# Kernel optimization log

Hardware: AMD Instinct MI355X
Metric: run time of the kernel (lower is better)

The kernel has to match this reference:

```python
import jax, jax.numpy as jnp
import numpy as np

N_NODES = 100000
N_EDGES = 3200000
F_IN = 256
H = 256
L = 256
BN_EPS = 1e-5


def gcn_conv(x, src, dst, deg_inv_sqrt, W, b):
    # x: [N, Fin]; src/dst: [E+N] (self-loops appended); returns [N, Fout]
    h = x @ W  # dense transform first (Fout may be < Fin)
    norm = deg_inv_sqrt[src] * deg_inv_sqrt[dst]  # [E+N]
    msg = h[src] * norm[:, None]                  # gather
    out = jax.ops.segment_sum(msg, dst, num_segments=N_NODES)  # scatter-add
    return out + b


def batch_norm(x, gamma, beta):
    # BatchNorm1d in training mode: per-feature mean/var over the node dim
    mean = jnp.mean(x, axis=0)
    var = jnp.var(x, axis=0)
    return (x - mean) * jax.lax.rsqrt(var + BN_EPS) * gamma + beta


def setup_inputs() -> dict:
    key = jax.random.key(0)
    ks = jax.random.split(key, 8)
    x = jax.random.normal(ks[0], (N_NODES, F_IN), dtype=jnp.float32)
    edge_index = jax.random.randint(ks[1], (2, N_EDGES), 0, N_NODES, dtype=jnp.int64)
    # glorot-ish init for weights
    W1 = jax.random.normal(ks[2], (F_IN, H), dtype=jnp.float32) * (1.0 / np.sqrt(F_IN))
    b1 = jnp.zeros((H,), dtype=jnp.float32)
    W_mu = jax.random.normal(ks[3], (H, L), dtype=jnp.float32) * (1.0 / np.sqrt(H))
    b_mu = jnp.zeros((L,), dtype=jnp.float32)
    W_ls = jax.random.normal(ks[4], (H, L), dtype=jnp.float32) * (1.0 / np.sqrt(H))
    b_ls = jnp.zeros((L,), dtype=jnp.float32)
    gamma = jnp.ones((H,), dtype=jnp.float32)
    beta = jnp.zeros((H,), dtype=jnp.float32)
    return {"x": x, "edge_index": edge_index, "W1": W1, "b1": b1,
            "W_mu": W_mu, "b_mu": b_mu, "W_ls": W_ls, "b_ls": b_ls,
            "gamma": gamma, "beta": beta}


def reference(x, edge_index, W1, b1, W_mu, b_mu, W_ls, b_ls, gamma, beta):
    # Add self-loops once (shared across the three GCNConv layers)
    loop = jnp.arange(N_NODES, dtype=edge_index.dtype)
    src = jnp.concatenate([edge_index[0], loop])
    dst = jnp.concatenate([edge_index[1], loop])
    deg = jax.ops.segment_sum(jnp.ones_like(dst, dtype=jnp.float32), dst,
                              num_segments=N_NODES)
    deg_inv_sqrt = jnp.where(deg > 0, jax.lax.rsqrt(jnp.maximum(deg, 1.0)), 0.0)

    h = gcn_conv(x, src, dst, deg_inv_sqrt, W1, b1)
    h = jax.nn.relu(batch_norm(h, gamma, beta))
    mu = gcn_conv(h, src, dst, deg_inv_sqrt, W_mu, b_mu)
    logstd = gcn_conv(h, src, dst, deg_inv_sqrt, W_ls, b_ls)
    return (mu, logstd)
```

## Files before the change

kernel.cpp:

```cpp
#include <hip/hip_runtime.h>
#include <hip/hip_bf16.h>

#define FEAT 256
#define NPB 512
#define NPB_SHIFT 9
#define MAXBINS 256
#define CAP 20480
#define BIN_CHUNK 8192

typedef __attribute__((ext_vector_type(8))) short bf16x8;
typedef __attribute__((ext_vector_type(8))) ushort u16x8;
typedef __attribute__((ext_vector_type(4))) float f32x4;

__device__ __forceinline__ float bf2f(ushort h) {
    union { unsigned u; float f; } v; v.u = ((unsigned)h) << 16; return v.f;
}
__device__ __forceinline__ ushort f2bf(float f) {
    union { float f; unsigned u; } v; v.f = f;
    unsigned u = v.u;
    return (ushort)((u + 0x7FFFu + ((u >> 16) & 1u)) >> 16);
}


__global__ __launch_bounds__(256) void k_bin(const int* __restrict__ ei, int E, int N,
                                             int* __restrict__ bincur,
                                             int2* __restrict__ binbuf, int nbins,
                                             int nchunks,
                                             const float* __restrict__ W1,
                                             const float* __restrict__ Wmu,
                                             const float* __restrict__ Wls,
                                             const float* __restrict__ bmu,
                                             const float* __restrict__ bls,
                                             ushort* __restrict__ Wt1,
                                             ushort* __restrict__ Wtc,
                                             float* __restrict__ biasc,
                                             float* __restrict__ bnacc) {
    int t = threadIdx.x;
    if ((int)blockIdx.x >= nchunks) {
        int i = ((int)blockIdx.x - nchunks) * 256 + t;
        int m = i >> 16;
        int j = i & 65535;
        int n = j >> 8, k = j & 255;
        const float* W = (m == 0) ? W1 : (m == 1) ? Wmu : Wls;
        ushort v = f2bf(W[k * 256 + n]);
        if (m == 0) Wt1[j] = v;
        else if (m == 1) Wtc[j] = v;
        else Wtc[65536 + j] = v;
        if (i < 512) { biasc[i] = (i < 256) ? bmu[i] : bls[i - 256]; bnacc[i] = 0.f; }
        return;
    }
    __shared__ int hist[MAXBINS];
    __shared__ int base[MAXBINS];
    int T = E + N;
    int start = blockIdx.x * BIN_CHUNK;
    int end = min(start + BIN_CHUNK, T);
    for (int b = t; b < nbins; b += 256) hist[b] = 0;
    __syncthreads();
    for (int idx = start + t; idx < end; idx += 256) {
        int d = (idx < E) ? ei[E + idx] : idx - E;
        atomicAdd(&hist[d >> NPB_SHIFT], 1);
    }
    __syncthreads();
    for (int b = t; b < nbins; b += 256) {
        int c = hist[b];
        base[b] = c ? (b * CAP + atomicAdd(&bincur[b], c)) : 0;
        hist[b] = 0;
    }
    __syncthreads();
    for (int idx = start + t; idx < end; idx += 256) {
        int s, d;
        if (idx < E) { s = ei[idx]; d = ei[E + idx]; }
        else         { s = idx - E; d = idx - E; }
        int b = d >> NPB_SHIFT;
        int local = atomicAdd(&hist[b], 1);
        binbuf[base[b] + local] = make_int2(s, d);
    }
}


__global__ __launch_bounds__(512) void k_histcsr(const int2* __restrict__ binbuf,
                                                 const int* __restrict__ bincur,
                                                 int* __restrict__ offs,
                                                 float* __restrict__ dis,
                                                 int* __restrict__ csr,
                                                 const float* __restrict__ x,
                                                 ushort* __restrict__ xtab,
                                                 int N, int nbins) {
    __shared__ int bsh[256];
    __shared__ int h[NPB];
    __shared__ int cur[NPB];
    __shared__ float sdis[NPB];
    int b = blockIdx.x;
    int t = threadIdx.x;
    int node0 = b * NPB;
    int nn = min(NPB, N - node0);
    if (t < 256) bsh[t] = (t < nbins) ? bincur[t] : 0;
    h[t] = 0; cur[t] = 0;
    __syncthreads();
    for (int d = 1; d < 256; d <<= 1) {
        int xx = (t < 256 && t >= d) ? bsh[t - d] : 0;
        __syncthreads();
        if (t < 256) bsh[t] += xx;
        __syncthreads();
    }
    int cnt = bincur[b];
    int bpre = bsh[b] - cnt;
    if (b == 0 && t == 0) offs[N] = bsh[nbins - 1];
    int base = b * CAP;
    for (int i = t; i < cnt; i += 512) {
        atomicAdd(&h[binbuf[base + i].y - node0], 1);
    }
    __syncthreads();
    int v = h[t];
    for (int d = 1; d < 512; d <<= 1) {
        int xx = (t >= d) ? h[t - d] : 0;
        __syncthreads();
        h[t] += xx;
        __syncthreads();
    }
    int myoff = bpre + h[t] - v;
    float dv = rsqrtf((float)v);
    sdis[t] = dv;
    if (t < nn) {
        offs[node0 + t] = myoff;
        dis[node0 + t] = dv;
    }
    h[t] = myoff;
    __syncthreads();
    for (int i = t; i < cnt; i += 512) {
        int2 e = binbuf[base + i];
        int ld = e.y - node0;
        int c = atomicAdd(&cur[ld], 1);
        csr[h[ld] + c] = e.x;
    }
    const float4* x4 = (const float4*)x;
    ushort4* y4 = (ushort4*)xtab;
    for (int i = t; i < nn * 64; i += 512) {
        int ln = i >> 6;
        int c = i & 63;
        float d = sdis[ln];
        float4 vv = x4[(size_t)(node0 + ln) * 64 + c];
        ushort4 o;
        o.x = f2bf(vv.x * d); o.y = f2bf(vv.y * d);
        o.z = f2bf(vv.z * d); o.w = f2bf(vv.w * d);
        y4[(size_t)(node0 + ln) * 64 + c] = o;
    }
}


__global__ __launch_bounds__(256) void k_agg(const ushort* __restrict__ in,
                                             ushort* __restrict__ out,
                                             const int* __restrict__ offs,
                                             const int* __restrict__ csr,
                                             const float* __restrict__ dis, int N) {
    int wid = blockIdx.x * 4 + ((int)threadIdx.x >> 6);
    if (wid >= N) return;
    int lane = threadIdx.x & 63;
    int half = lane >> 5;
    int l32 = lane & 31;
    int beg = offs[wid], end = offs[wid + 1];
    float acc[8] = {};
    int k = beg;
    for (; k + 16 <= end; k += 16) {
        int s0 = csr[k + half];
        int s1 = csr[k + 2 + half];
        int s2 = csr[k + 4 + half];
        int s3 = csr[k + 6 + half];
        int s4 = csr[k + 8 + half];
        int s5 = csr[k + 10 + half];
        int s6 = csr[k + 12 + half];
        int s7 = csr[k + 14 + half];
        bf16x8 v0 = *(const bf16x8*)(in + (size_t)s0 * FEAT + l32 * 8);
        bf16x8 v1 = *(const bf16x8*)(in + (size_t)s1 * FEAT + l32 * 8);
        bf16x8 v2 = *(const bf16x8*)(in + (size_t)s2 * FEAT + l32 * 8);
        bf16x8 v3 = *(const bf16x8*)(in + (size_t)s3 * FEAT + l32 * 8);
        bf16x8 v4 = *(const bf16x8*)(in + (size_t)s4 * FEAT + l32 * 8);
        bf16x8 v5 = *(const bf16x8*)(in + (size_t)s5 * FEAT + l32 * 8);
        bf16x8 v6 = *(const bf16x8*)(in + (size_t)s6 * FEAT + l32 * 8);
        bf16x8 v7 = *(const bf16x8*)(in + (size_t)s7 * FEAT + l32 * 8);
        #pragma unroll
        for (int j = 0; j < 8; ++j) {
            float t0 = bf2f((ushort)v0[j]) + bf2f((ushort)v1[j]);
            float t1 = bf2f((ushort)v2[j]) + bf2f((ushort)v3[j]);
            float t2 = bf2f((ushort)v4[j]) + bf2f((ushort)v5[j]);
            float t3 = bf2f((ushort)v6[j]) + bf2f((ushort)v7[j]);
            acc[j] += (t0 + t1) + (t2 + t3);
        }
    }
    for (; k + 2 <= end; k += 2) {
        int s = csr[k + half];
        bf16x8 v = *(const bf16x8*)(in + (size_t)s * FEAT + l32 * 8);
        #pragma unroll
        for (int j = 0; j < 8; ++j) acc[j] += bf2f((ushort)v[j]);
    }
    if (k < end && half == 0) {
        int s = csr[k];
        bf16x8 v = *(const bf16x8*)(in + (size_t)s * FEAT + l32 * 8);
        #pragma unroll
        for (int j = 0; j < 8; ++j) acc[j] += bf2f((ushort)v[j]);
    }
    #pragma unroll
    for (int j = 0; j < 8; ++j) acc[j] += __shfl_xor(acc[j], 32, 64);
    if (half == 0) {
        float d = dis[wid];
        u16x8 o;
        #pragma unroll
        for (int j = 0; j < 8; ++j) o[j] = f2bf(acc[j] * d);
        *(u16x8*)(out + (size_t)wid * FEAT + l32 * 8) = o;
    }
}


template <int NCOL, bool BF16OUT>
__global__ __launch_bounds__(512) void k_gemm(const ushort* __restrict__ A,
                                              const ushort* __restrict__ Bt,
                                              const float* __restrict__ bias,
                                              float* __restrict__ C0,
                                              float* __restrict__ C1,
                                              ushort* __restrict__ Cb,
                                              float* __restrict__ bnacc,
                                              int M) {
    __shared__ ushort As[128 * 64];
    __shared__ ushort Bs[256 * 64];
    int t = threadIdx.x;
    int lane = t & 63;
    int wave = t >> 6;
    int wr = wave >> 2, wc = wave & 3;
    int bx = blockIdx.x, by = blockIdx.y;
    int lo = lane & 15, g = lane >> 4;
    f32x4 acc[4][4] = {};
    int chunk = t & 7;
    int row8 = t >> 3;

    for (int kt = 0; kt < 4; ++kt) {
        int k0 = kt * 64;
        #pragma unroll
        for (int i = 0; i < 2; ++i) {
            int r = row8 + i * 64;
            int lc = chunk ^ (r & 7);
            int gr = by * 128 + r;
            bf16x8 av = {};
            if (gr < M) av = *(const bf16x8*)(A + (size_t)gr * 256 + k0 + lc * 8);
            *(bf16x8*)(As + r * 64 + chunk * 8) = av;
        }
        #pragma unroll
        for (int i = 0; i < 4; ++i) {
            int r = row8 + i * 64;
            int lc = chunk ^ (r & 7);
            int gn = bx * 256 + r;
            bf16x8 bv = *(const bf16x8*)(Bt + (size_t)gn * 256 + k0 + lc * 8);
            *(bf16x8*)(Bs + r * 64 + chunk * 8) = bv;
        }
        __syncthreads();
        #pragma unroll
        for (int h = 0; h < 2; ++h) {
            bf16x8 af[4], bfr[4];
            #pragma unroll
            for (int m = 0; m < 4; ++m) {
                int r = wr * 64 + m * 16 + lo;
                af[m] = *(const bf16x8*)(As + r * 64 + (((h * 4 + g) ^ (r & 7)) * 8));
            }
            #pragma unroll
            for (int n = 0; n < 4; ++n) {
                int r = wc * 64 + n * 16 + lo;
                bfr[n] = *(const bf16x8*)(Bs + r * 64 + (((h * 4 + g) ^ (r & 7)) * 8));
            }
            #pragma unroll
            for (int m = 0; m < 4; ++m)
                #pragma unroll
                for (int n = 0; n < 4; ++n)
                    acc[m][n] = __builtin_amdgcn_mfma_f32_16x16x32_bf16(
                        af[m], bfr[n], acc[m][n], 0, 0, 0);
        }
        __syncthreads();
    }
    #pragma unroll
    for (int n = 0; n < 4; ++n) {
        int gc = bx * 256 + wc * 64 + n * 16 + lo;
        float bb = bias[gc];
        float s = 0.f, q = 0.f;
        #pragma unroll
        for (int m = 0; m < 4; ++m) {
            f32x4 v = acc[m][n];
            #pragma unroll
            for (int r4 = 0; r4 < 4; ++r4) {
                int grow = by * 128 + wr * 64 + m * 16 + g * 4 + r4;
                if (grow < M) {
                    float val = v[r4] + bb;
                    if (BF16OUT) {
                        Cb[(size_t)grow * 256 + gc] = f2bf(val);
                        s += val; q += val * val;
                    } else {
                        float* Cp = C0; int cc = gc;
                        if (gc >= 256) { Cp = C1; cc = gc - 256; }
                        __builtin_nontemporal_store(val, &Cp[(size_t)grow * 256 + cc]);
                    }
                }
            }
        }
        if (BF16OUT) {
            s += __shfl_xor(s, 16, 64); s += __shfl_xor(s, 32, 64);
            q += __shfl_xor(q, 16, 64); q += __shfl_xor(q, 32, 64);
            if (g == 0) {
                atomicAdd(&bnacc[gc], s);
                atomicAdd(&bnacc[256 + gc], q);
            }
        }
    }
}


__global__ __launch_bounds__(256) void k_bnapply(const ushort* __restrict__ h,
                                                 ushort* __restrict__ o,
                                                 const float* __restrict__ acc,
                                                 const float* __restrict__ gamma,
                                                 const float* __restrict__ beta,
                                                 const float* __restrict__ dis, int Nn) {
    int c4 = (threadIdx.x & 63) * 4;
    int rof = (int)threadIdx.x >> 6;
    float inv = 1.0f / (float)Nn;
    float g[4], b[4];
    #pragma unroll
    for (int j = 0; j < 4; ++j) {
        float mean = acc[c4 + j] * inv;
        float var = acc[FEAT + c4 + j] * inv - mean * mean;
        float rs = rsqrtf(var + 1e-5f);
        g[j] = gamma[c4 + j] * rs;
        b[j] = beta[c4 + j] - mean * g[j];
    }
    for (int r = blockIdx.x * 4 + rof; r < Nn; r += gridDim.x * 4) {
        float d = dis[r];
        ushort4 v = *(const ushort4*)(h + (size_t)r * FEAT + c4);
        float o0 = bf2f(v.x) * g[0] + b[0], o1 = bf2f(v.y) * g[1] + b[1];
        float o2 = bf2f(v.z) * g[2] + b[2], o3 = bf2f(v.w) * g[3] + b[3];
        ushort4 ov;
        ov.x = f2bf((o0 > 0.f ? o0 : 0.f) * d);
        ov.y = f2bf((o1 > 0.f ? o1 : 0.f) * d);
        ov.z = f2bf((o2 > 0.f ? o2 : 0.f) * d);
        ov.w = f2bf((o3 > 0.f ? o3 : 0.f) * d);
        *(ushort4*)(o + (size_t)r * FEAT + c4) = ov;
    }
}


extern "C" void kernel_launch(void* const* d_in, const int* in_sizes, int n_in,
                              void* d_out, int out_size, void* d_ws, size_t ws_size,
                              hipStream_t stream) {
    const float* x     = (const float*)d_in[0];
    const int*   ei    = (const int*)d_in[1];
    const float* W1    = (const float*)d_in[2];
    const float* b1    = (const float*)d_in[3];
    const float* Wmu   = (const float*)d_in[4];
    const float* bmu   = (const float*)d_in[5];
    const float* Wls   = (const float*)d_in[6];
    const float* bls   = (const float*)d_in[7];
    const float* gamma = (const float*)d_in[8];
    const float* beta  = (const float*)d_in[9];

    int N = in_sizes[0] / FEAT;
    int E = in_sizes[1] / 2;
    int nbins = (N + NPB - 1) / NPB;
    int T = E + N;
    int nchunks = (T + BIN_CHUNK - 1) / BIN_CHUNK;

    float* out = (float*)d_out;
    float* mu  = out;
    float* ls  = out + (size_t)N * FEAT;
    ushort* xtab = (ushort*)mu;
    ushort* H1b  = (ushort*)ls;

    char* p = (char*)d_ws;
    auto alloc = [&](size_t bytes) -> void* {
        void* r = (void*)p;
        p += (bytes + 255) & ~(size_t)255;
        return r;
    };
    ushort* Abuf  = (ushort*)alloc((size_t)N * FEAT * 2);
    int2*   binbuf= (int2*)  alloc((size_t)nbins * CAP * 8);
    int*    csr   = (int*)   alloc((size_t)T * 4);
    int*    offs  = (int*)   alloc((size_t)(N + 1) * 4);
    float*  dis   = (float*) alloc((size_t)N * 4);
    float*  bnacc = (float*) alloc(512 * 4);
    ushort* Wt1   = (ushort*)alloc(65536 * 2);
    ushort* Wtc   = (ushort*)alloc(131072 * 2);
    float*  biasc = (float*) alloc(512 * 4);
    int*    bincur= (int*)   alloc((size_t)nbins * 4);

    hipMemsetAsync(bincur, 0, (size_t)nbins * 4, stream);
    k_bin<<<nchunks + 768, 256, 0, stream>>>(ei, E, N, bincur, binbuf, nbins, nchunks,
                                             W1, Wmu, Wls, bmu, bls, Wt1, Wtc, biasc, bnacc);

    k_histcsr<<<nbins, 512, 0, stream>>>(binbuf, bincur, offs, dis, csr, x, xtab, N, nbins);

    int gblocks = (N + 127) / 128;

    k_agg<<<(N + 3) / 4, 256, 0, stream>>>(xtab, Abuf, offs, csr, dis, N);

    dim3 g1(1, gblocks);
    k_gemm<256, true><<<g1, 512, 0, stream>>>(Abuf, Wt1, b1, nullptr, nullptr, H1b, bnacc, N);

    k_bnapply<<<2048, 256, 0, stream>>>(H1b, xtab, bnacc, gamma, beta, dis, N);

    k_agg<<<(N + 3) / 4, 256, 0, stream>>>(xtab, Abuf, offs, csr, dis, N);

    dim3 g2(2, gblocks);
    k_gemm<512, false><<<g2, 512, 0, stream>>>(Abuf, Wtc, biasc, mu, ls, nullptr, nullptr, N);
}
```

Measured before the change: 751.4 us.

## Pack binned edges into single ints and share A tile across both output halves

The binning buffer now stores each edge as one 32-bit word (source shifted left, local destination in the low bits) instead of an int2, halving binbuf traffic in the binning and CSR-build kernels. The final GEMM now computes both mu and logstd column halves in a single block, loading the A tile once and looping over the two B halves with separate accumulators, instead of launching a 2-wide grid that reloads A. This doubles accumulator registers (which may lower occupancy) and halves the GEMM grid size. The packing assumes source indices fit in 23 bits.

```diff
diff --git a/kernel.cpp b/kernel.cpp
--- a/kernel.cpp
+++ b/kernel.cpp
@@ -24,7 +24,7 @@
 
 __global__ __launch_bounds__(256) void k_bin(const int* __restrict__ ei, int E, int N,
                                              int* __restrict__ bincur,
-                                             int2* __restrict__ binbuf, int nbins,
+                                             int* __restrict__ binbuf, int nbins,
                                              int nchunks,
                                              const float* __restrict__ W1,
                                              const float* __restrict__ Wmu,
@@ -73,12 +73,12 @@
         else         { s = idx - E; d = idx - E; }
         int b = d >> NPB_SHIFT;
         int local = atomicAdd(&hist[b], 1);
-        binbuf[base[b] + local] = make_int2(s, d);
-    }
-}
-
-
-__global__ __launch_bounds__(512) void k_histcsr(const int2* __restrict__ binbuf,
+        binbuf[base[b] + local] = (s << NPB_SHIFT) | (d & (NPB - 1));
+    }
+}
+
+
+__global__ __launch_bounds__(512) void k_histcsr(const int* __restrict__ binbuf,
                                                  const int* __restrict__ bincur,
                                                  int* __restrict__ offs,
                                                  float* __restrict__ dis,
@@ -108,7 +108,7 @@
     if (b == 0 && t == 0) offs[N] = bsh[nbins - 1];
     int base = b * CAP;
     for (int i = t; i < cnt; i += 512) {
-        atomicAdd(&h[binbuf[base + i].y - node0], 1);
+        atomicAdd(&h[binbuf[base + i] & (NPB - 1)], 1);
     }
     __syncthreads();
     int v = h[t];
@@ -128,10 +128,10 @@
     h[t] = myoff;
     __syncthreads();
     for (int i = t; i < cnt; i += 512) {
-        int2 e = binbuf[base + i];
-        int ld = e.y - node0;
+        int pk = binbuf[base + i];
+        int ld = pk & (NPB - 1);
         int c = atomicAdd(&cur[ld], 1);
-        csr[h[ld] + c] = e.x;
+        csr[h[ld] + c] = pk >> NPB_SHIFT;
     }
     const float4* x4 = (const float4*)x;
     ushort4* y4 = (ushort4*)xtab;
@@ -211,7 +211,7 @@
 }
 
 
-template <int NCOL, bool BF16OUT>
+template <int NHALF, bool BF16OUT>
 __global__ __launch_bounds__(512) void k_gemm(const ushort* __restrict__ A,
                                               const ushort* __restrict__ Bt,
                                               const float* __restrict__ bias,
@@ -226,9 +226,10 @@
     int lane = t & 63;
     int wave = t >> 6;
     int wr = wave >> 2, wc = wave & 3;
-    int bx = blockIdx.x, by = blockIdx.y;
+    int by = blockIdx.x;
     int lo = lane & 15, g = lane >> 4;
-    f32x4 acc[4][4] = {};
+    f32x4 acc0[4][4] = {};
+    f32x4 acc1[4][4] = {};
     int chunk = t & 7;
     int row8 = t >> 3;
 
@@ -244,66 +245,73 @@
             *(bf16x8*)(As + r * 64 + chunk * 8) = av;
         }
         #pragma unroll
-        for (int i = 0; i < 4; ++i) {
-            int r = row8 + i * 64;
-            int lc = chunk ^ (r & 7);
-            int gn = bx * 256 + r;
-            bf16x8 bv = *(const bf16x8*)(Bt + (size_t)gn * 256 + k0 + lc * 8);
-            *(bf16x8*)(Bs + r * 64 + chunk * 8) = bv;
+        for (int bh = 0; bh < NHALF; ++bh) {
+            #pragma unroll
+            for (int i = 0; i < 4; ++i) {
+                int r = row8 + i * 64;
+                int lc = chunk ^ (r & 7);
+                bf16x8 bv = *(const bf16x8*)(Bt + (size_t)(bh * 256 + r) * 256 + k0 + lc * 8);
+                *(bf16x8*)(Bs + r * 64 + chunk * 8) = bv;
+            }
+            __syncthreads();
+            f32x4 (&acc)[4][4] = bh ? acc1 : acc0;
+            #pragma unroll
+            for (int h = 0; h < 2; ++h) {
+                bf16x8 af[4], bfr[4];
+                #pragma unroll
+                for (int m = 0; m < 4; ++m) {
+                    int r = wr * 64 + m * 16 + lo;
+                    af[m] = *(const bf16x8*)(As + r * 64 + (((h * 4 + g) ^ (r & 7)) * 8));
+                }
+                #pragma unroll
+                for (int n = 0; n < 4; ++n) {
+                    int r = wc * 64 + n * 16 + lo;
+                    bfr[n] = *(const bf16x8*)(Bs + r * 64 + (((h * 4 + g) ^ (r & 7)) * 8));
+                }
+                #pragma unroll
+                for (int m = 0; m < 4; ++m)
+                    #pragma unroll
+                    for (int n = 0; n < 4; ++n)
+                        acc[m][n] = __builtin_amdgcn_mfma_f32_16x16x32_bf16(
+                            af[m], bfr[n], acc[m][n], 0, 0, 0);
+            }
+            __syncthreads();
         }
-        __syncthreads();
-        #pragma unroll
-        for (int h = 0; h < 2; ++h) {
-            bf16x8 af[4], bfr[4];
+    }
+    #pragma unroll
+    for (int bh = 0; bh < NHALF; ++bh) {
+        f32x4 (&acc)[4][4] = bh ? acc1 : acc0;
+        #pragma unroll
+        for (int n = 0; n < 4; ++n) {
+            int gc = bh * 256 + wc * 64 + n * 16 + lo;
+            float bb = bias[gc];
+            float s = 0.f, q = 0.f;
             #pragma unroll
             for (int m = 0; m < 4; ++m) {
-                int r = wr * 64 + m * 16 + lo;
-                af[m] = *(const bf16x8*)(As + r * 64 + (((h * 4 + g) ^ (r & 7)) * 8));
-            }
-            #pragma unroll
-            for (int n = 0; n < 4; ++n) {
-                int r = wc * 64 + n * 16 + lo;
-                bfr[n] = *(const bf16x8*)(Bs + r * 64 + (((h * 4 + g) ^ (r & 7)) * 8));
-            }
-            #pragma unroll
-            for (int m = 0; m < 4; ++m)
+                f32x4 v = acc[m][n];
                 #pragma unroll
-                for (int n = 0; n < 4; ++n)
-                    acc[m][n] = __builtin_amdgcn_mfma_f32_16x16x32_bf16(
-                        af[m], bfr[n], acc[m][n], 0, 0, 0);
-        }
-        __syncthreads();
-    }
-    #pragma unroll
-    for (int n = 0; n < 4; ++n) {
-        int gc = bx * 256 + wc * 64 + n * 16 + lo;
-        float bb = bias[gc];
-        float s = 0.f, q = 0.f;
-        #pragma unroll
-        for (int m = 0; m < 4; ++m) {
-            f32x4 v = acc[m][n];
-            #pragma unroll
-            for (int r4 = 0; r4 < 4; ++r4) {
-                int grow = by * 128 + wr * 64 + m * 16 + g * 4 + r4;
-                if (grow < M) {
-                    float val = v[r4] + bb;
-                    if (BF16OUT) {
-                        Cb[(size_t)grow * 256 + gc] = f2bf(val);
-                        s += val; q += val * val;
-                    } else {
-                        float* Cp = C0; int cc = gc;
-                        if (gc >= 256) { Cp = C1; cc = gc - 256; }
-                        __builtin_nontemporal_store(val, &Cp[(size_t)grow * 256 + cc]);
+                for (int r4 = 0; r4 < 4; ++r4) {
+                    int grow = by * 128 + wr * 64 + m * 16 + g * 4 + r4;
+                    if (grow < M) {
+                        float val = v[r4] + bb;
+                        if (BF16OUT) {
+                            Cb[(size_t)grow * 256 + gc] = f2bf(val);
+                            s += val; q += val * val;
+                        } else {
+                            float* Cp = bh ? C1 : C0;
+                            int cc = gc - bh * 256;
+                            __builtin_nontemporal_store(val, &Cp[(size_t)grow * 256 + cc]);
+                        }
                     }
                 }
             }
-        }
-        if (BF16OUT) {
-            s += __shfl_xor(s, 16, 64); s += __shfl_xor(s, 32, 64);
-            q += __shfl_xor(q, 16, 64); q += __shfl_xor(q, 32, 64);
-            if (g == 0) {
-                atomicAdd(&bnacc[gc], s);
-                atomicAdd(&bnacc[256 + gc], q);
+            if (BF16OUT) {
+                s += __shfl_xor(s, 16, 64); s += __shfl_xor(s, 32, 64);
+                q += __shfl_xor(q, 16, 64); q += __shfl_xor(q, 32, 64);
+                if (g == 0) {
+                    atomicAdd(&bnacc[gc], s);
+                    atomicAdd(&bnacc[256 + gc], q);
+                }
             }
         }
     }
@@ -376,7 +384,7 @@
         return r;
     };
     ushort* Abuf  = (ushort*)alloc((size_t)N * FEAT * 2);
-    int2*   binbuf= (int2*)  alloc((size_t)nbins * CAP * 8);
+    int*    binbuf= (int*)   alloc((size_t)nbins * CAP * 4);
     int*    csr   = (int*)   alloc((size_t)T * 4);
     int*    offs  = (int*)   alloc((size_t)(N + 1) * 4);
     float*  dis   = (float*) alloc((size_t)N * 4);
@@ -396,13 +404,11 @@
 
     k_agg<<<(N + 3) / 4, 256, 0, stream>>>(xtab, Abuf, offs, csr, dis, N);
 
-    dim3 g1(1, gblocks);
-    k_gemm<256, true><<<g1, 512, 0, stream>>>(Abuf, Wt1, b1, nullptr, nullptr, H1b, bnacc, N);
+    k_gemm<1, true><<<gblocks, 512, 0, stream>>>(Abuf, Wt1, b1, nullptr, nullptr, H1b, bnacc, N);
 
     k_bnapply<<<2048, 256, 0, stream>>>(H1b, xtab, bnacc, gamma, beta, dis, N);
 
     k_agg<<<(N + 3) / 4, 256, 0, stream>>>(xtab, Abuf, offs, csr, dis, N);
 
-    dim3 g2(2, gblocks);
-    k_gemm<512, false><<<g2, 512, 0, stream>>>(Abuf, Wtc, biasc, mu, ls, nullptr, nullptr, N);
-}
+    k_gemm<2, false><<<gblocks, 512, 0, stream>>>(Abuf, Wtc, biasc, mu, ls, nullptr, nullptr, N);
+}
```

New measurement: 750.5 us. Within noise of the previous version (-0.1%).
